# Kernel optimization log

Hardware: AMD Instinct MI355X
Metric: run time of the kernel (lower is better)

## Reference

```python
import jax, jax.numpy as jnp
import numpy as np

N_BITS = 8
QMAX = float(2 ** (N_BITS - 1) - 1)   # 127
QMIN = -QMAX - 1.0                     # -128
EPS = 1e-8


def _fq(x, scale):
    # symmetric fake quant: round, clamp, dequant
    return jnp.clip(jnp.round(x / scale), QMIN, QMAX) * scale


def fake_quant_per_token(x):
    # one scale per [..., :] vector (amax over last dim)
    max_abs = jnp.max(jnp.abs(x), axis=-1, keepdims=True)
    scale = jnp.maximum(max_abs / QMAX, EPS)
    return _fq(x, scale)


def fake_quant_per_channel(w):
    # w: [out, in]; ch_axis=0 -> one scale per output row (reduce over dim 1)
    max_abs = jnp.max(jnp.abs(w), axis=1, keepdims=True)
    scale = jnp.maximum(max_abs / QMAX, EPS)
    return _fq(w, scale)


def setup_inputs() -> dict:
    key = jax.random.key(0)
    kx, kw, kb = jax.random.split(key, 3)
    B, S, D_IN, D_OUT = 4, 2048, 4096, 4096
    x = jax.random.normal(kx, (B, S, D_IN), dtype=jnp.float32)
    w = jax.random.normal(kw, (D_OUT, D_IN), dtype=jnp.float32) * 0.02
    b = jax.random.normal(kb, (D_OUT,), dtype=jnp.float32) * 0.02
    return {"x": x, "w": w, "b": b}


def reference(x, w, b):
    # fake-quant path: W8 per-channel weight, A8 per-token activation
    w_q = fake_quant_per_channel(w)           # [O, I]
    x_q = fake_quant_per_token(x)             # [B, S, I]
    y = jnp.einsum('bsi,oi->bso', x_q, w_q) + b
    return y
```

## Files before the change

### kernel.cpp

```cpp
#include <hip/hip_runtime.h>
#include <hip/hip_bf16.h>


#define K_DIM 4096
#define N_DIM 4096

typedef int v4i __attribute__((ext_vector_type(4)));

__device__ __forceinline__ void cp16(void* lds, const void* g) {
    __builtin_amdgcn_global_load_lds(
        (const __attribute__((address_space(1))) void*)g,
        (__attribute__((address_space(3))) void*)lds, 16, 0, 0);
}

__global__ __launch_bounds__(256) void quant_rows_kernel(
    const float* __restrict__ x, const float* __restrict__ w, int M,
    char* __restrict__ qx, char* __restrict__ qw,
    float* __restrict__ sx, float* __restrict__ sw) {
    const int blk = blockIdx.x;
    const bool is_x = blk < M;
    const int row = is_x ? blk : blk - M;
    const float* rp = (is_x ? x : w) + (size_t)row * 4096;
    char* qdst = is_x ? qx : qw;
    float* sdst = is_x ? sx : sw;

    const int tid = threadIdx.x;

    float4 v[4];
#pragma unroll
    for (int i = 0; i < 4; ++i)
        v[i] = *(const float4*)(rp + 4 * (tid + 256 * i));

    float m = 0.0f;
#pragma unroll
    for (int i = 0; i < 4; ++i) {
        m = fmaxf(m, fmaxf(fmaxf(fabsf(v[i].x), fabsf(v[i].y)),
                           fmaxf(fabsf(v[i].z), fabsf(v[i].w))));
    }
#pragma unroll
    for (int off = 32; off > 0; off >>= 1)
        m = fmaxf(m, __shfl_down(m, off));

    __shared__ float red[4];
    if ((tid & 63) == 0) red[tid >> 6] = m;
    __syncthreads();
    const float amax = fmaxf(fmaxf(red[0], red[1]), fmaxf(red[2], red[3]));
    const float scale = fmaxf(amax / 127.0f, 1e-8f);

    int* qout = (int*)(qdst + (size_t)row * 4096);
#pragma unroll
    for (int i = 0; i < 4; ++i) {
        int q0 = (int)fminf(fmaxf(rintf(v[i].x / scale), -128.0f), 127.0f);
        int q1 = (int)fminf(fmaxf(rintf(v[i].y / scale), -128.0f), 127.0f);
        int q2 = (int)fminf(fmaxf(rintf(v[i].z / scale), -128.0f), 127.0f);
        int q3 = (int)fminf(fmaxf(rintf(v[i].w / scale), -128.0f), 127.0f);
        qout[tid + 256 * i] =
            (q0 & 255) | ((q1 & 255) << 8) | ((q2 & 255) << 16) | ((q3 & 255) << 24);
    }
    if (tid == 0) sdst[row] = scale;
}

__global__ __launch_bounds__(256) void gemm_i8_kernel(
    const char* __restrict__ qx, const char* __restrict__ qw,
    const float* __restrict__ sx, const float* __restrict__ sw,
    const float* __restrict__ bias, float* __restrict__ y) {

    __shared__ __align__(16) char As[128 * 64];
    __shared__ __align__(16) char Bs[128 * 64];

    const int tid = threadIdx.x;
    const int wave = tid >> 6;
    const int lane = tid & 63;
    const int ln = lane & 15;
    const int lg = lane >> 4;
    const int wm = wave & 1;
    const int wn = wave >> 1;

    const int bm = blockIdx.y;
    const int bn = blockIdx.x;

    const char* aBase = qx + (size_t)bm * 128 * K_DIM;
    const char* bBase = qw + (size_t)bn * 128 * K_DIM;

    const int c0 = tid;
    const int c1 = tid + 256;
    const int r0 = c0 >> 2;
    const int r1 = c1 >> 2;
    const int kc0 = (c0 & 3) ^ ((c0 >> 3) & 3);
    const int kc1 = (c1 & 3) ^ ((c1 >> 3) & 3);

    v4i acc[4][4] = {};

    const int kxor = (lg ^ ((ln >> 1) & 3)) << 4;
    int aOff[4], bOff[4];
#pragma unroll
    for (int t = 0; t < 4; ++t) {
        aOff[t] = (wm * 64 + t * 16 + ln) * 64 + kxor;
        bOff[t] = (wn * 64 + t * 16 + ln) * 64 + kxor;
    }

    for (int k0 = 0; k0 < K_DIM; k0 += 64) {
        cp16(As + c0 * 16, aBase + (size_t)r0 * K_DIM + k0 + kc0 * 16);
        cp16(As + c1 * 16, aBase + (size_t)r1 * K_DIM + k0 + kc1 * 16);
        cp16(Bs + c0 * 16, bBase + (size_t)r0 * K_DIM + k0 + kc0 * 16);
        cp16(Bs + c1 * 16, bBase + (size_t)r1 * K_DIM + k0 + kc1 * 16);
        __syncthreads();

        v4i afr[4], bfr[4];
#pragma unroll
        for (int t = 0; t < 4; ++t) afr[t] = *(const v4i*)(As + aOff[t]);
#pragma unroll
        for (int t = 0; t < 4; ++t) bfr[t] = *(const v4i*)(Bs + bOff[t]);

#pragma unroll
        for (int mt = 0; mt < 4; ++mt)
#pragma unroll
            for (int nt = 0; nt < 4; ++nt)
                acc[mt][nt] = __builtin_amdgcn_mfma_i32_16x16x64_i8(
                    afr[mt], bfr[nt], acc[mt][nt], 0, 0, 0);

        __syncthreads();
    }

    const int m_base = bm * 128 + wm * 64;
    const int n_base = bn * 128 + wn * 64;

    float sxr[4][4];
#pragma unroll
    for (int mt = 0; mt < 4; ++mt)
#pragma unroll
        for (int r = 0; r < 4; ++r)
            sxr[mt][r] = sx[m_base + mt * 16 + lg * 4 + r];

#pragma unroll
    for (int nt = 0; nt < 4; ++nt) {
        const int n = n_base + nt * 16 + ln;
        const float swv = sw[n];
        const float bv = bias[n];
#pragma unroll
        for (int mt = 0; mt < 4; ++mt) {
            const int row = m_base + mt * 16 + lg * 4;
#pragma unroll
            for (int r = 0; r < 4; ++r) {
                y[(size_t)(row + r) * N_DIM + n] =
                    (float)acc[mt][nt][r] * sxr[mt][r] * swv + bv;
            }
        }
    }
}

extern "C" void kernel_launch(void* const* d_in, const int* in_sizes, int n_in,
                              void* d_out, int out_size, void* d_ws, size_t ws_size,
                              hipStream_t stream) {
    const float* x = (const float*)d_in[0];
    const float* w = (const float*)d_in[1];
    const float* b = (const float*)d_in[2];
    float* y = (float*)d_out;

    const int M = in_sizes[0] / K_DIM;
    const int O = in_sizes[1] / K_DIM;

    char* qx = (char*)d_ws;
    char* qw = qx + (size_t)M * K_DIM;
    float* sx = (float*)(qw + (size_t)O * K_DIM);
    float* sw = sx + M;

    quant_rows_kernel<<<M + O, 256, 0, stream>>>(x, w, M, qx, qw, sx, sw);

    dim3 grid(N_DIM / 128, M / 128);
    gemm_i8_kernel<<<grid, 256, 0, stream>>>(qx, qw, sx, sw, b, y);
}
```

Before: 428.7 us.

## Rework int8 GEMM into 256x256 tiles with double-buffered async LDS pipeline

The GEMM grows from 128x128 tiles with 4 waves to 256x256 tiles with 8 waves and a K-step of 128, using 128 KB of LDS as two parity buffers. Global-to-LDS loads for the next A and B tiles are issued in the middle of the current tile's MFMA phases, with manual vmcnt waits, barriers and setprio to overlap memory with compute. A XOR swizzle across 8 chunks avoids LDS bank conflicts. This cuts global traffic per FLOP and hides load latency, but the grid shrinks to 16x32 blocks with fewer waves in flight, and register pressure rises.

```diff
diff --git a/kernel.cpp b/kernel.cpp
--- a/kernel.cpp
+++ b/kernel.cpp
@@ -4,6 +4,7 @@
 
 #define K_DIM 4096
 #define N_DIM 4096
+#define NT (K_DIM / 128)
 
 typedef int v4i __attribute__((ext_vector_type(4)));
 
@@ -60,93 +61,171 @@
     if (tid == 0) sdst[row] = scale;
 }
 
-__global__ __launch_bounds__(256) void gemm_i8_kernel(
+__global__ __launch_bounds__(512, 2) void gemm_i8_kernel(
     const char* __restrict__ qx, const char* __restrict__ qw,
     const float* __restrict__ sx, const float* __restrict__ sw,
     const float* __restrict__ bias, float* __restrict__ y) {
 
-    __shared__ __align__(16) char As[128 * 64];
-    __shared__ __align__(16) char Bs[128 * 64];
-
-    const int tid = threadIdx.x;
+    __shared__ __align__(16) char lds[131072];
+
+    const int tid  = threadIdx.x;
     const int wave = tid >> 6;
     const int lane = tid & 63;
-    const int ln = lane & 15;
-    const int lg = lane >> 4;
-    const int wm = wave & 1;
-    const int wn = wave >> 1;
+    const int ln   = lane & 15;
+    const int lg   = lane >> 4;
+    const int wm   = wave >> 2;
+    const int wn   = wave & 3;
 
     const int bm = blockIdx.y;
     const int bn = blockIdx.x;
 
-    const char* aBase = qx + (size_t)bm * 128 * K_DIM;
-    const char* bBase = qw + (size_t)bn * 128 * K_DIM;
-
-    const int c0 = tid;
-    const int c1 = tid + 256;
-    const int r0 = c0 >> 2;
-    const int r1 = c1 >> 2;
-    const int kc0 = (c0 & 3) ^ ((c0 >> 3) & 3);
-    const int kc1 = (c1 & 3) ^ ((c1 >> 3) & 3);
-
-    v4i acc[4][4] = {};
-
-    const int kxor = (lg ^ ((ln >> 1) & 3)) << 4;
-    int aOff[4], bOff[4];
-#pragma unroll
-    for (int t = 0; t < 4; ++t) {
-        aOff[t] = (wm * 64 + t * 16 + ln) * 64 + kxor;
-        bOff[t] = (wn * 64 + t * 16 + ln) * 64 + kxor;
-    }
-
-    for (int k0 = 0; k0 < K_DIM; k0 += 64) {
-        cp16(As + c0 * 16, aBase + (size_t)r0 * K_DIM + k0 + kc0 * 16);
-        cp16(As + c1 * 16, aBase + (size_t)r1 * K_DIM + k0 + kc1 * 16);
-        cp16(Bs + c0 * 16, bBase + (size_t)r0 * K_DIM + k0 + kc0 * 16);
-        cp16(Bs + c1 * 16, bBase + (size_t)r1 * K_DIM + k0 + kc1 * 16);
-        __syncthreads();
-
+    const int ci0 = tid,       r0s = ci0 >> 3, c0s = (ci0 & 7) ^ (r0s & 7);
+    const int ci1 = tid + 512, r1s = ci1 >> 3, c1s = (ci1 & 7) ^ (r1s & 7);
+    const char* aS0 = qx + (size_t)(bm * 256 + r0s) * K_DIM + c0s * 16;
+    const char* aS1 = qx + (size_t)(bm * 256 + r1s) * K_DIM + c1s * 16;
+    const char* bS0 = qw + (size_t)(bn * 256 + r0s) * K_DIM + c0s * 16;
+    const char* bS1 = qw + (size_t)(bn * 256 + r1s) * K_DIM + c1s * 16;
+    const int ldsC0 = ci0 * 16, ldsC1 = ci1 * 16;
+
+#define SLOT_A(par, h) ((par) * 65536 + (h) * 16384)
+#define SLOT_B(par, h) ((par) * 65536 + 32768 + (h) * 16384)
+#define STAGE_A(par, h, t) do {                                              \
+    cp16(lds + SLOT_A(par, h) + ldsC0,                                       \
+         aS0 + (size_t)(h) * 128 * K_DIM + (size_t)(t) * 128);               \
+    cp16(lds + SLOT_A(par, h) + ldsC1,                                       \
+         aS1 + (size_t)(h) * 128 * K_DIM + (size_t)(t) * 128); } while (0)
+#define STAGE_B(par, h, t) do {                                              \
+    cp16(lds + SLOT_B(par, h) + ldsC0,                                       \
+         bS0 + (size_t)(h) * 128 * K_DIM + (size_t)(t) * 128);               \
+    cp16(lds + SLOT_B(par, h) + ldsC1,                                       \
+         bS1 + (size_t)(h) * 128 * K_DIM + (size_t)(t) * 128); } while (0)
+
+    const int ch0 = (lg ^ (ln & 7)) * 16;
+    const int ch1 = ch0 ^ 64;
+    const int aRd = wm * 16384 + ln * 128;
+    const int bRd = 32768 + (wn >> 1) * 16384 + ((wn & 1) * 64 + ln) * 128;
+
+    v4i acc[8][4] = {};
+
+    STAGE_A(0, 0, 0); STAGE_A(0, 1, 0);
+    STAGE_B(0, 0, 0); STAGE_B(0, 1, 0);
+    STAGE_B(1, 0, 1); STAGE_B(1, 1, 1);
+    asm volatile("s_waitcnt vmcnt(4)" ::: "memory");
+    __builtin_amdgcn_s_barrier();
+    asm volatile("" ::: "memory");
+
+    for (int t = 0; t < NT; ++t) {
+        const int par  = t & 1;
+        const int base = par * 65536;
         v4i afr[4], bfr[4];
-#pragma unroll
-        for (int t = 0; t < 4; ++t) afr[t] = *(const v4i*)(As + aOff[t]);
-#pragma unroll
-        for (int t = 0; t < 4; ++t) bfr[t] = *(const v4i*)(Bs + bOff[t]);
-
-#pragma unroll
-        for (int mt = 0; mt < 4; ++mt)
-#pragma unroll
-            for (int nt = 0; nt < 4; ++nt)
-                acc[mt][nt] = __builtin_amdgcn_mfma_i32_16x16x64_i8(
-                    afr[mt], bfr[nt], acc[mt][nt], 0, 0, 0);
-
-        __syncthreads();
-    }
-
-    const int m_base = bm * 128 + wm * 64;
-    const int n_base = bn * 128 + wn * 64;
-
-    float sxr[4][4];
-#pragma unroll
-    for (int mt = 0; mt < 4; ++mt)
+
+#pragma unroll
+        for (int m = 0; m < 4; ++m)
+            afr[m] = *(const v4i*)(lds + base + aRd + m * 2048 + ch0);
+#pragma unroll
+        for (int n = 0; n < 4; ++n)
+            bfr[n] = *(const v4i*)(lds + base + bRd + n * 2048 + ch0);
+        if (t + 1 < NT) STAGE_A(par ^ 1, 0, t + 1);
+        __builtin_amdgcn_s_barrier();
+        asm volatile("" ::: "memory");
+        __builtin_amdgcn_s_setprio(1);
+#pragma unroll
+        for (int m = 0; m < 4; ++m)
+#pragma unroll
+            for (int n = 0; n < 4; ++n)
+                acc[m][n] = __builtin_amdgcn_mfma_i32_16x16x64_i8(
+                    afr[m], bfr[n], acc[m][n], 0, 0, 0);
+        __builtin_amdgcn_s_setprio(0);
+        __builtin_amdgcn_s_barrier();
+        asm volatile("" ::: "memory");
+
+#pragma unroll
+        for (int m = 0; m < 4; ++m)
+            afr[m] = *(const v4i*)(lds + base + aRd + (4 + m) * 2048 + ch0);
+        if (t + 1 < NT) STAGE_A(par ^ 1, 1, t + 1);
+        __builtin_amdgcn_s_barrier();
+        asm volatile("" ::: "memory");
+        __builtin_amdgcn_s_setprio(1);
+#pragma unroll
+        for (int m = 0; m < 4; ++m)
+#pragma unroll
+            for (int n = 0; n < 4; ++n)
+                acc[4 + m][n] = __builtin_amdgcn_mfma_i32_16x16x64_i8(
+                    afr[m], bfr[n], acc[4 + m][n], 0, 0, 0);
+        __builtin_amdgcn_s_setprio(0);
+        __builtin_amdgcn_s_barrier();
+        asm volatile("" ::: "memory");
+
+#pragma unroll
+        for (int m = 0; m < 4; ++m)
+            afr[m] = *(const v4i*)(lds + base + aRd + m * 2048 + ch1);
+#pragma unroll
+        for (int n = 0; n < 4; ++n)
+            bfr[n] = *(const v4i*)(lds + base + bRd + n * 2048 + ch1);
+        __builtin_amdgcn_s_barrier();
+        asm volatile("" ::: "memory");
+        __builtin_amdgcn_s_setprio(1);
+#pragma unroll
+        for (int m = 0; m < 4; ++m)
+#pragma unroll
+            for (int n = 0; n < 4; ++n)
+                acc[m][n] = __builtin_amdgcn_mfma_i32_16x16x64_i8(
+                    afr[m], bfr[n], acc[m][n], 0, 0, 0);
+        __builtin_amdgcn_s_setprio(0);
+        __builtin_amdgcn_s_barrier();
+        asm volatile("" ::: "memory");
+
+#pragma unroll
+        for (int m = 0; m < 4; ++m)
+            afr[m] = *(const v4i*)(lds + base + aRd + (4 + m) * 2048 + ch1);
+        if (t + 2 < NT) { STAGE_B(par, 0, t + 2); STAGE_B(par, 1, t + 2); }
+        __builtin_amdgcn_s_barrier();
+        asm volatile("" ::: "memory");
+        __builtin_amdgcn_s_setprio(1);
+#pragma unroll
+        for (int m = 0; m < 4; ++m)
+#pragma unroll
+            for (int n = 0; n < 4; ++n)
+                acc[4 + m][n] = __builtin_amdgcn_mfma_i32_16x16x64_i8(
+                    afr[m], bfr[n], acc[4 + m][n], 0, 0, 0);
+        __builtin_amdgcn_s_setprio(0);
+        if (t + 2 < NT)
+            asm volatile("s_waitcnt vmcnt(4)" ::: "memory");
+        else
+            asm volatile("s_waitcnt vmcnt(0)" ::: "memory");
+        __builtin_amdgcn_s_barrier();
+        asm volatile("" ::: "memory");
+    }
+
+    const int m_base = bm * 256 + wm * 128;
+    const int n_base = bn * 256 + wn * 64;
+
+    float sxr[8][4];
+#pragma unroll
+    for (int m = 0; m < 8; ++m)
 #pragma unroll
         for (int r = 0; r < 4; ++r)
-            sxr[mt][r] = sx[m_base + mt * 16 + lg * 4 + r];
-
-#pragma unroll
-    for (int nt = 0; nt < 4; ++nt) {
-        const int n = n_base + nt * 16 + ln;
-        const float swv = sw[n];
-        const float bv = bias[n];
-#pragma unroll
-        for (int mt = 0; mt < 4; ++mt) {
-            const int row = m_base + mt * 16 + lg * 4;
+            sxr[m][r] = sx[m_base + m * 16 + lg * 4 + r];
+
+#pragma unroll
+    for (int n = 0; n < 4; ++n) {
+        const int col = n_base + n * 16 + ln;
+        const float swv = sw[col];
+        const float bv  = bias[col];
+#pragma unroll
+        for (int m = 0; m < 8; ++m) {
+            const int row = m_base + m * 16 + lg * 4;
 #pragma unroll
             for (int r = 0; r < 4; ++r) {
-                y[(size_t)(row + r) * N_DIM + n] =
-                    (float)acc[mt][nt][r] * sxr[mt][r] * swv + bv;
+                y[(size_t)(row + r) * N_DIM + col] =
+                    (float)acc[m][n][r] * sxr[m][r] * swv + bv;
             }
         }
     }
+#undef SLOT_A
+#undef SLOT_B
+#undef STAGE_A
+#undef STAGE_B
 }
 
 extern "C" void kernel_launch(void* const* d_in, const int* in_sizes, int n_in,
@@ -167,6 +246,6 @@
 
     quant_rows_kernel<<<M + O, 256, 0, stream>>>(x, w, M, qx, qw, sx, sw);
 
-    dim3 grid(N_DIM / 128, M / 128);
-    gemm_i8_kernel<<<grid, 256, 0, stream>>>(qx, qw, sx, sw, b, y);
-}
+    dim3 grid(N_DIM / 256, M / 256);
+    gemm_i8_kernel<<<grid, 512, 0, stream>>>(qx, qw, sx, sw, b, y);
+}
```

Result: faster. 385.9 us (-10.0%).
